# Optimization experiments

Hardware: AMD Instinct MI355X
Metric: run time of the kernel (lower is better)

## Reference

```python
import jax, jax.numpy as jnp
import numpy as np

HID, H, D = 128, 4, 32
NB, NP, NC = 60000, 2000, 4000
EM, EP, EI = 150000, 300000, 150000


def segment_softmax(logits, seg, n):
    # logits: [E, H], seg: [E] destination ids
    m = jax.ops.segment_max(logits, seg, num_segments=n)
    m = jnp.where(jnp.isfinite(m), m, 0.0)  # guard empty segments
    e = jnp.exp(logits - m[seg])
    s = jax.ops.segment_sum(e, seg, num_segments=n)
    return e / (s[seg] + 1e-16)


def layer_norm(x, g, b):
    mu = x.mean(-1, keepdims=True)
    v = ((x - mu) ** 2).mean(-1, keepdims=True)
    return (x - mu) / jnp.sqrt(v + 1e-5) * g + b


def setup_inputs():
    key = jax.random.key(0)
    ks = jax.random.split(key, 40)
    i = iter(range(40))
    nrm = lambda shape, s=1.0: jax.random.normal(ks[next(i)], shape, jnp.float32) * s
    w = lambda shape: nrm(shape, 0.05)
    inp = {
        'x_ball': nrm((NB, HID)),
        'x_player': nrm((NP, HID)),
        'x_context': nrm((NC, HID)),
        'em': jnp.stack([jax.random.randint(ks[next(i)], (EM,), 0, NP),
                         jax.random.randint(ks[next(i)], (EM,), 0, NB)]),
        'ep': jnp.stack([jax.random.randint(ks[next(i)], (EP,), 0, NB),
                         jax.random.randint(ks[next(i)], (EP,), 0, NB)]),
        'ei': jnp.stack([jax.random.randint(ks[next(i)], (EI,), 0, NB),
                         jax.random.randint(ks[next(i)], (EI,), 0, NC)]),
        'ea_p': nrm((EP, 1)),
        # GATv2Conv (player -matchup-> ball)
        'g_Wl': w((HID, HID)), 'g_Wr': w((HID, HID)), 'g_att': w((H, D)), 'g_b': jnp.zeros((HID,), jnp.float32),
        # TransformerConv (ball -recent_precedes-> ball), edge_dim=1
        't_Wq': w((HID, HID)), 't_bq': jnp.zeros((HID,), jnp.float32),
        't_Wk': w((HID, HID)), 't_bk': jnp.zeros((HID,), jnp.float32),
        't_Wv': w((HID, HID)), 't_bv': jnp.zeros((HID,), jnp.float32),
        't_We': w((1, HID)),
        't_Wskip': w((HID, HID)), 't_bskip': jnp.zeros((HID,), jnp.float32),
        # SAGEConv mean (ball -informs-> context)
        's_Wl': w((HID, HID)), 's_bl': jnp.zeros((HID,), jnp.float32), 's_Wr': w((HID, HID)),
        # per-type LayerNorms (only applied to types produced by the conv)
        'ln_ball_g': jnp.ones((HID,), jnp.float32), 'ln_ball_b': jnp.zeros((HID,), jnp.float32),
        'ln_ctx_g': jnp.ones((HID,), jnp.float32), 'ln_ctx_b': jnp.zeros((HID,), jnp.float32),
    }
    return inp


def reference(x_ball, x_player, x_context, em, ep, ei, ea_p,
              g_Wl, g_Wr, g_att, g_b,
              t_Wq, t_bq, t_Wk, t_bk, t_Wv, t_bv, t_We, t_Wskip, t_bskip,
              s_Wl, s_bl, s_Wr,
              ln_ball_g, ln_ball_b, ln_ctx_g, ln_ctx_b):
    # ---- GATv2Conv: player -> ball ----
    src, dst = em[0], em[1]
    xl = (x_player @ g_Wl).reshape(NP, H, D)   # src transform
    xr = (x_ball @ g_Wr).reshape(NB, H, D)     # dst transform
    e = xl[src] + xr[dst]                      # [EM, H, D]
    e = jnp.where(e > 0, e, 0.2 * e)           # leaky_relu(0.2)
    logit = jnp.einsum('ehd,hd->eh', e, g_att)
    alpha = segment_softmax(logit, dst, NB)
    gat = jax.ops.segment_sum(xl[src] * alpha[..., None], dst, num_segments=NB)
    gat = gat.reshape(NB, HID) + g_b

    # ---- TransformerConv: ball -> ball, edge_dim=1 ----
    src, dst = ep[0], ep[1]
    q = (x_ball @ t_Wq + t_bq).reshape(NB, H, D)
    k = (x_ball @ t_Wk + t_bk).reshape(NB, H, D)
    v = (x_ball @ t_Wv + t_bv).reshape(NB, H, D)
    ee = (ea_p @ t_We).reshape(EP, H, D)       # lin_edge (no bias)
    kj = k[src] + ee
    logit = jnp.einsum('ehd,ehd->eh', q[dst], kj) / jnp.sqrt(jnp.float32(D))
    alpha = segment_softmax(logit, dst, NB)
    tr = jax.ops.segment_sum((v[src] + ee) * alpha[..., None], dst, num_segments=NB)
    tr = tr.reshape(NB, HID) + x_ball @ t_Wskip + t_bskip  # root/skip connection

    # ---- SAGEConv mean: ball -> context ----
    src, dst = ei[0], ei[1]
    summ = jax.ops.segment_sum(x_ball[src], dst, num_segments=NC)
    cnt = jax.ops.segment_sum(jnp.ones((EI,), jnp.float32), dst, num_segments=NC)
    mean = summ / jnp.maximum(cnt, 1.0)[:, None]
    sage = mean @ s_Wl + s_bl + x_context @ s_Wr

    # ---- HeteroConv aggr='sum' + residual + per-type LayerNorm ----
    ball_out = layer_norm(gat + tr + x_ball, ln_ball_g, ln_ball_b)
    ctx_out = layer_norm(sage + x_context, ln_ctx_g, ln_ctx_b)
    # 'player' receives no messages -> passed through unchanged
    return (ball_out, ctx_out, x_player)
```

## Files before the change

### kernel.cpp

```cpp
#include <hip/hip_runtime.h>
#include <hip/hip_bf16.h>

#define NB 60000
#define NP 2000
#define NC 4000
#define EM_N 150000
#define EP_N 300000
#define EI_N 150000
#define POOL_N (EM_N + EP_N + EI_N)
#define SEG_TOT (NB + NB + NC)
#define SCAN_BLK 1024
#define NPART ((SEG_TOT + SCAN_BLK - 1) / SCAN_BLK)
#define BALL_BLKS ((NB + 127) / 128)
#define PLYR_BLKS ((NP + 127) / 128)
#define GEMM_BLKS (BALL_BLKS + PLYR_BLKS)
#define FILL_BLKS ((POOL_N + 255) / 256)
#define COPY_BLKS ((NP * 128 + 255) / 256)
#define BBALL ((NB + 3) / 4)
#define CTX_BLKS ((NC + 15) / 16)

typedef __hip_bfloat16 bf16;
typedef unsigned int u32;
typedef __attribute__((ext_vector_type(8))) short s8v;
typedef __attribute__((ext_vector_type(4))) float f4v;

__device__ __forceinline__ short f2bs(float f) {
    bf16 h = __float2bfloat16(f);
    return __builtin_bit_cast(short, h);
}
__device__ __forceinline__ float bsToF(short s) {
    return __builtin_bit_cast(float, ((unsigned)(unsigned short)s) << 16);
}
__device__ __forceinline__ float loF(u32 v) { return bsToF((short)(v & 0xffff)); }
__device__ __forceinline__ float hiF(u32 v) { return bsToF((short)(v >> 16)); }
__device__ __forceinline__ u32 packbf(float a, float b) {
    return (u32)(unsigned short)f2bs(a) | ((u32)(unsigned short)f2bs(b) << 16);
}

__global__ void hist_wt_copy_kernel(const int* __restrict__ em, const int* __restrict__ ep,
                                    const int* __restrict__ ei, int* __restrict__ counts,
                                    const float* __restrict__ W0, const float* __restrict__ W1,
                                    const float* __restrict__ W2, const float* __restrict__ W3,
                                    const float* __restrict__ W4, const float* __restrict__ W5,
                                    ushort* __restrict__ Wt,
                                    const float* __restrict__ x_player, float* __restrict__ out) {
    if (blockIdx.x >= FILL_BLKS) {
        int t = (blockIdx.x - FILL_BLKS) * 256 + threadIdx.x;
        if (t < NP * 128) out[(size_t)(NB + NC) * 128 + t] = x_player[t];
        return;
    }
    int t = blockIdx.x * 256 + threadIdx.x;
    if (t < 6 * 16384) {
        int w = t >> 14, r = t & 16383, k = r >> 7, n = r & 127;
        const float* W = (w == 0) ? W0 : (w == 1) ? W1 : (w == 2) ? W2 : (w == 3) ? W3
                       : (w == 4) ? W4 : W5;
        int sc = (n >> 5) * 32 + ((n & 1) << 4) + ((n & 31) >> 1);
        Wt[w * 16384 + sc * 128 + k] = (unsigned short)f2bs(W[k * 128 + n]);
    }
    if (t < EM_N) atomicAdd(&counts[em[EM_N + t]], 1);
    else if (t < EM_N + EP_N) atomicAdd(&counts[NB + ep[EP_N + (t - EM_N)]], 1);
    else if (t < POOL_N) atomicAdd(&counts[2 * NB + ei[EI_N + (t - EM_N - EP_N)]], 1);
}

__global__ void scan_fused_kernel(const int* __restrict__ counts, int* __restrict__ offsets,
                                  int* __restrict__ cursors, int* __restrict__ gbase) {
    __shared__ int sd[256];
    __shared__ int sbase;
    int b = blockIdx.x, tid = threadIdx.x;
    int base = b * SCAN_BLK + tid * 4;
    int v[4]; int ts = 0;
#pragma unroll
    for (int j = 0; j < 4; j++) { int idx = base + j; v[j] = (idx < SEG_TOT) ? counts[idx] : 0; ts += v[j]; }
    sd[tid] = ts;
    for (int off = 1; off < 256; off <<= 1) {
        __syncthreads(); int t = (tid >= off) ? sd[tid - off] : 0;
        __syncthreads(); sd[tid] += t;
    }
    __syncthreads();
    if (tid == 255) sbase = atomicAdd(gbase, sd[255]);
    __syncthreads();
    int run = sd[tid] - ts + sbase;
#pragma unroll
    for (int j = 0; j < 4; j++) {
        int idx = base + j;
        if (idx < SEG_TOT) { offsets[idx] = run; cursors[idx] = run; }
        run += v[j];
    }
}

__global__ __launch_bounds__(256) void gemm6_fill_kernel(
    const float* __restrict__ Aball, const float* __restrict__ Aplyr,
    const ushort* __restrict__ Wt,
    const float* __restrict__ bq, const float* __restrict__ bk,
    const float* __restrict__ bv_, const float* __restrict__ bskip,
    const float* __restrict__ g_b,
    u32* __restrict__ xrP, u32* __restrict__ qP, u32* __restrict__ kvP,
    u32* __restrict__ skipP, u32* __restrict__ xlP,
    const int* __restrict__ em, const int* __restrict__ ep, const int* __restrict__ ei,
    const float* __restrict__ ea_p, int* __restrict__ cursors, int2* __restrict__ pool) {
    if (blockIdx.x >= GEMM_BLKS) {
        int t = (blockIdx.x - GEMM_BLKS) * 256 + threadIdx.x;
        int seg, s; float ea = 0.f;
        if (t < EM_N) { s = em[t]; seg = em[EM_N + t]; }
        else if (t < EM_N + EP_N) { int e = t - EM_N; s = ep[e]; seg = NB + ep[EP_N + e]; ea = ea_p[e]; }
        else if (t < POOL_N) { int e = t - EM_N - EP_N; s = ei[e]; seg = 2 * NB + ei[EI_N + e]; }
        else return;
        int pos = atomicAdd(&cursors[seg], 1);
        pool[pos] = make_int2(s, __float_as_int(ea));
        return;
    }
    const int lane = threadIdx.x & 63;
    const int wv = threadIdx.x >> 6;
    const int quad = lane >> 4, l16 = lane & 15;
    const bool plyr = (blockIdx.x >= BALL_BLKS);
    const int M = plyr ? NP : NB;
    const float* A = plyr ? Aplyr : Aball;
    const int mbase = (plyr ? (blockIdx.x - BALL_BLKS) : blockIdx.x) * 128 + wv * 32;

    s8v a[2][4];
#pragma unroll
    for (int mt = 0; mt < 2; mt++) {
        int row = mbase + mt * 16 + l16;
        if (row >= M) row = M - 1;
        const float* ap = A + (size_t)row * 128 + quad * 8;
#pragma unroll
        for (int kt = 0; kt < 4; kt++) {
            const float4* p = (const float4*)(ap + kt * 32);
            float4 u = p[0], v = p[1];
            s8v f;
            f[0] = f2bs(u.x); f[1] = f2bs(u.y); f[2] = f2bs(u.z); f[3] = f2bs(u.w);
            f[4] = f2bs(v.x); f[5] = f2bs(v.y); f[6] = f2bs(v.z); f[7] = f2bs(v.w);
            a[mt][kt] = f;
        }
    }

    const int wbeg = plyr ? 5 : 0, wend = plyr ? 6 : 5;
    for (int w = wbeg; w < wend; w++) {
        const ushort* wt = Wt + w * 16384;
        u32* op; const float* bp; int stride, obase;
        if (w == 0)      { op = xrP;   bp = nullptr; stride = 64;  obase = 0; }
        else if (w == 1) { op = qP;    bp = bq;      stride = 64;  obase = 0; }
        else if (w == 2) { op = kvP;   bp = bk;      stride = 128; obase = 0; }
        else if (w == 3) { op = kvP;   bp = bv_;     stride = 128; obase = 1; }
        else if (w == 4) { op = skipP; bp = bskip;   stride = 64;  obase = 0; }
        else             { op = xlP;   bp = nullptr; stride = 64;  obase = 0; }
        const int kvmul = (stride == 128) ? 2 : 1;
        const bool resid = (w == 4);
#pragma unroll
        for (int t = 0; t < 4; t++) {
            s8v blo[4], bhi[4];
#pragma unroll
            for (int kt = 0; kt < 4; kt++) {
                blo[kt] = *(const s8v*)(wt + (t * 32 + l16) * 128 + kt * 32 + quad * 8);
                bhi[kt] = *(const s8v*)(wt + (t * 32 + 16 + l16) * 128 + kt * 32 + quad * 8);
            }
            float bvlo = 0.f, bvhi = 0.f;
            if (bp) { float2 b2 = ((const float2*)bp)[t * 16 + l16]; bvlo = b2.x; bvhi = b2.y; }
            if (resid) { float2 gb2 = ((const float2*)g_b)[t * 16 + l16]; bvlo += gb2.x; bvhi += gb2.y; }
#pragma unroll
            for (int mt = 0; mt < 2; mt++) {
                f4v alo = {0.f, 0.f, 0.f, 0.f}, ahi = {0.f, 0.f, 0.f, 0.f};
#pragma unroll
                for (int kt = 0; kt < 4; kt++) {
                    alo = __builtin_amdgcn_mfma_f32_16x16x32_bf16(a[mt][kt], blo[kt], alo, 0, 0, 0);
                    ahi = __builtin_amdgcn_mfma_f32_16x16x32_bf16(a[mt][kt], bhi[kt], ahi, 0, 0, 0);
                }
#pragma unroll
                for (int r = 0; r < 4; r++) {
                    int row = mbase + mt * 16 + quad * 4 + r;
                    if (row < M) {
                        float vlo = alo[r] + bvlo, vhi = ahi[r] + bvhi;
                        if (resid) {
                            float2 xr2 = ((const float2*)Aball)[(size_t)row * 64 + t * 16 + l16];
                            vlo += xr2.x; vhi += xr2.y;
                        }
                        op[(size_t)row * stride + (t * 16 + l16) * kvmul + obase] = packbf(vlo, vhi);
                    }
                }
            }
        }
    }
}

__global__ __launch_bounds__(256) void ball_sage_kernel(
    const u32* __restrict__ xlP, const u32* __restrict__ xrP, const u32* __restrict__ qP,
    const u32* __restrict__ kvP, const u32* __restrict__ skipP,
    const float* __restrict__ x_ball,
    const float* __restrict__ g_att, const float* __restrict__ We,
    const int* __restrict__ offsets, const int* __restrict__ counts,
    const int2* __restrict__ pool,
    const float* __restrict__ ln_g, const float* __restrict__ ln_b,
    float* __restrict__ summ, float* __restrict__ out) {
    __shared__ float part[4][128];
    const int wv = threadIdx.x >> 6, l = threadIdx.x & 63;

    if (blockIdx.x >= BBALL) {
        int c = blockIdx.x - BBALL;
        int beg = offsets[2 * NB + c], cnt = counts[2 * NB + c];
        float s0 = 0.f, s1 = 0.f;
        for (int j = wv; j < cnt; j += 4) {
            int s = pool[beg + j].x;
            float2 xv = ((const float2*)x_ball)[(size_t)s * 64 + l];
            s0 += xv.x; s1 += xv.y;
        }
        part[wv][l * 2] = s0; part[wv][l * 2 + 1] = s1;
        __syncthreads();
        if (wv == 0) {
            float m = fmaxf((float)cnt, 1.f);
            size_t rowC = (size_t)c * 128;
            summ[rowC + l * 2] = (part[0][l * 2] + part[1][l * 2] + part[2][l * 2] + part[3][l * 2]) / m;
            summ[rowC + l * 2 + 1] =
                (part[0][l * 2 + 1] + part[1][l * 2 + 1] + part[2][l * 2 + 1] + part[3][l * 2 + 1]) / m;
        }
        return;
    }

    const int d = blockIdx.x * 4 + wv;
    if (d >= NB) return;
    const size_t rowD = (size_t)d * 64;

    float2 att = ((const float2*)g_att)[l];
    u32 xr2 = xrP[rowD + l];
    float xr0 = loF(xr2), xr1 = hiF(xr2);
    int beg = offsets[d], cnt = counts[d];
    float n0 = 0.f, n1 = 0.f, deg = 0.f;
    int j = 0;
    for (; j + 3 < cnt; j += 4) {
        int s0 = pool[beg + j].x, s1 = pool[beg + j + 1].x;
        int s2 = pool[beg + j + 2].x, s3 = pool[beg + j + 3].x;
        u32 xv[4] = {xlP[(size_t)s0 * 64 + l], xlP[(size_t)s1 * 64 + l],
                     xlP[(size_t)s2 * 64 + l], xlP[(size_t)s3 * 64 + l]};
        float p[4], xa[4], xb[4];
#pragma unroll
        for (int i = 0; i < 4; i++) {
            xa[i] = loF(xv[i]); xb[i] = hiF(xv[i]);
            float u0 = xa[i] + xr0; u0 = u0 > 0.f ? u0 : 0.2f * u0;
            float u1 = xb[i] + xr1; u1 = u1 > 0.f ? u1 : 0.2f * u1;
            p[i] = u0 * att.x + u1 * att.y;
        }
#pragma unroll
        for (int m = 1; m <= 8; m <<= 1) {
#pragma unroll
            for (int i = 0; i < 4; i++) p[i] += __shfl_xor(p[i], m);
        }
#pragma unroll
        for (int i = 0; i < 4; i++) {
            p[i] = __expf(p[i]);
            n0 += p[i] * xa[i]; n1 += p[i] * xb[i]; deg += p[i];
        }
    }
    for (; j < cnt; j++) {
        int s = pool[beg + j].x;
        u32 xv = xlP[(size_t)s * 64 + l];
        float x0 = loF(xv), x1 = hiF(xv);
        float u0 = x0 + xr0; u0 = u0 > 0.f ? u0 : 0.2f * u0;
        float u1 = x1 + xr1; u1 = u1 > 0.f ? u1 : 0.2f * u1;
        float p = u0 * att.x + u1 * att.y;
#pragma unroll
        for (int m = 1; m <= 8; m <<= 1) p += __shfl_xor(p, m);
        p = __expf(p);
        n0 += p * x0; n1 += p * x1; deg += p;
    }
    float gat0 = n0 / (deg + 1e-16f), gat1 = n1 / (deg + 1e-16f);

    u32 q2 = qP[rowD + l];
    float q0 = loF(q2), q1 = hiF(q2);
    float2 we = ((const float2*)We)[l];
    float dw = q0 * we.x + q1 * we.y;
#pragma unroll
    for (int m = 1; m <= 8; m <<= 1) dw += __shfl_xor(dw, m);
    beg = offsets[NB + d]; cnt = counts[NB + d];
    float sv0 = 0.f, sv1 = 0.f, spe = 0.f, det = 0.f;
    const uint2* kv2p = (const uint2*)kvP;
    j = 0;
    for (; j + 3 < cnt; j += 4) {
        int2 pr[4] = {pool[beg + j], pool[beg + j + 1], pool[beg + j + 2], pool[beg + j + 3]};
        uint2 kv[4];
#pragma unroll
        for (int i = 0; i < 4; i++) kv[i] = kv2p[(size_t)pr[i].x * 64 + l];
        float p[4], ea[4];
#pragma unroll
        for (int i = 0; i < 4; i++) {
            ea[i] = __int_as_float(pr[i].y);
            p[i] = q0 * loF(kv[i].x) + q1 * hiF(kv[i].x);
        }
#pragma unroll
        for (int m = 1; m <= 8; m <<= 1) {
#pragma unroll
            for (int i = 0; i < 4; i++) p[i] += __shfl_xor(p[i], m);
        }
#pragma unroll
        for (int i = 0; i < 4; i++) {
            p[i] = __expf((p[i] + ea[i] * dw) * 0.17677669529663687f);
            sv0 += p[i] * loF(kv[i].y); sv1 += p[i] * hiF(kv[i].y);
            spe += p[i] * ea[i]; det += p[i];
        }
    }
    for (; j < cnt; j++) {
        int2 pr = pool[beg + j];
        float ea = __int_as_float(pr.y);
        uint2 kv = kv2p[(size_t)pr.x * 64 + l];
        float p = q0 * loF(kv.x) + q1 * hiF(kv.x);
#pragma unroll
        for (int m = 1; m <= 8; m <<= 1) p += __shfl_xor(p, m);
        p = __expf((p + ea * dw) * 0.17677669529663687f);
        sv0 += p * loF(kv.y); sv1 += p * hiF(kv.y);
        spe += p * ea; det += p;
    }
    float tr0 = (sv0 + spe * we.x) / (det + 1e-16f);
    float tr1 = (sv1 + spe * we.y) / (det + 1e-16f);

    u32 sk = skipP[rowD + l];
    float val0 = loF(sk) + gat0 + tr0;
    float val1 = hiF(sk) + gat1 + tr1;
    float s = val0 + val1;
#pragma unroll
    for (int m = 1; m <= 32; m <<= 1) s += __shfl_xor(s, m);
    float mu = s * (1.f / 128.f);
    float d0 = val0 - mu, d1 = val1 - mu;
    float qv = d0 * d0 + d1 * d1;
#pragma unroll
    for (int m = 1; m <= 32; m <<= 1) qv += __shfl_xor(qv, m);
    float inv = rsqrtf(qv * (1.f / 128.f) + 1e-5f);
    float2 g2 = ((const float2*)ln_g)[l];
    float2 b2 = ((const float2*)ln_b)[l];
    ((float2*)out)[rowD + l] = make_float2(d0 * inv * g2.x + b2.x, d1 * inv * g2.y + b2.y);
}

__global__ void ctx_fused_kernel(const float* __restrict__ xc, const float* __restrict__ summ,
                                 const float* __restrict__ Wr, const float* __restrict__ Wl,
                                 const float* __restrict__ bl,
                                 const float* __restrict__ g, const float* __restrict__ b,
                                 float* __restrict__ out) {
    __shared__ float A0[16 * 128];
    __shared__ float A1[16 * 128];
    __shared__ float CB[16 * 128];
    const int tid = threadIdx.x;
    const int row0 = blockIdx.x * 16;
    for (int i = tid; i < 16 * 128; i += 256) {
        int r = row0 + (i >> 7);
        A0[i] = (r < NC) ? xc[(size_t)r * 128 + (i & 127)] : 0.f;
        A1[i] = (r < NC) ? summ[(size_t)r * 128 + (i & 127)] : 0.f;
    }
    __syncthreads();
    const int col = tid & 127, rg = tid >> 7;
    float acc[8];
#pragma unroll
    for (int i = 0; i < 8; i++) acc[i] = 0.f;
    for (int k = 0; k < 128; k++) {
        float w0 = Wr[k * 128 + col], w1 = Wl[k * 128 + col];
#pragma unroll
        for (int i = 0; i < 8; i++)
            acc[i] += A0[(rg * 8 + i) * 128 + k] * w0 + A1[(rg * 8 + i) * 128 + k] * w1;
    }
    float bv = bl[col];
#pragma unroll
    for (int i = 0; i < 8; i++)
        CB[(rg * 8 + i) * 128 + col] = acc[i] + bv + A0[(rg * 8 + i) * 128 + col];
    __syncthreads();
    const int wv = tid >> 6, l = tid & 63;
    for (int r = 0; r < 4; r++) {
        int lr = wv * 4 + r, row = row0 + lr;
        if (row >= NC) break;
        float v0 = CB[lr * 128 + l], v1 = CB[lr * 128 + l + 64];
        float s = v0 + v1;
#pragma unroll
        for (int m = 1; m <= 32; m <<= 1) s += __shfl_xor(s, m);
        float mu = s * (1.f / 128.f);
        float d0 = v0 - mu, d1 = v1 - mu;
        float qv = d0 * d0 + d1 * d1;
#pragma unroll
        for (int m = 1; m <= 32; m <<= 1) qv += __shfl_xor(qv, m);
        float inv = rsqrtf(qv * (1.f / 128.f) + 1e-5f);
        out[(size_t)row * 128 + l] = d0 * inv * g[l] + b[l];
        out[(size_t)row * 128 + l + 64] = d1 * inv * g[l + 64] + b[l + 64];
    }
}

extern "C" void kernel_launch(void* const* d_in, const int* in_sizes, int n_in,
                              void* d_out, int out_size, void* d_ws, size_t ws_size,
                              hipStream_t stream) {
    const float* x_ball = (const float*)d_in[0];
    const float* x_player = (const float*)d_in[1];
    const float* x_context = (const float*)d_in[2];
    const int* em = (const int*)d_in[3];
    const int* ep = (const int*)d_in[4];
    const int* ei = (const int*)d_in[5];
    const float* ea_p = (const float*)d_in[6];
    const float* g_Wl = (const float*)d_in[7];
    const float* g_Wr = (const float*)d_in[8];
    const float* g_att = (const float*)d_in[9];
    const float* g_b = (const float*)d_in[10];
    const float* t_Wq = (const float*)d_in[11];
    const float* t_bq = (const float*)d_in[12];
    const float* t_Wk = (const float*)d_in[13];
    const float* t_bk = (const float*)d_in[14];
    const float* t_Wv = (const float*)d_in[15];
    const float* t_bv = (const float*)d_in[16];
    const float* t_We = (const float*)d_in[17];
    const float* t_Wskip = (const float*)d_in[18];
    const float* t_bskip = (const float*)d_in[19];
    const float* s_Wl = (const float*)d_in[20];
    const float* s_bl = (const float*)d_in[21];
    const float* s_Wr = (const float*)d_in[22];
    const float* ln_ball_g = (const float*)d_in[23];
    const float* ln_ball_b = (const float*)d_in[24];
    const float* ln_ctx_g = (const float*)d_in[25];
    const float* ln_ctx_b = (const float*)d_in[26];
    float* out = (float*)d_out;

    float* ws = (float*)d_ws;
    size_t o = 0;
    float* summ = ws + o;           o += (size_t)NC * 128;
    int* counts = (int*)(ws + o);   o += SEG_TOT;
    int* gbase = (int*)(ws + o);    o += 1;
    int* offsets = (int*)(ws + o);  o += SEG_TOT;
    int* cursors = (int*)(ws + o);  o += SEG_TOT;
    if (o & 1) o++;
    int2* pool = (int2*)(ws + o);   o += (size_t)POOL_N * 2;
    ushort* Wt = (ushort*)(ws + o); o += (6 * 16384) / 2;
    u32* xlP = (u32*)(ws + o);      o += (size_t)NP * 64;
    u32* xrP = (u32*)(ws + o);      o += (size_t)NB * 64;
    u32* qP = (u32*)(ws + o);       o += (size_t)NB * 64;
    u32* skipP = (u32*)(ws + o);    o += (size_t)NB * 64;
    if (o & 1) o++;
    u32* kvP = (u32*)(ws + o);      o += (size_t)NB * 128;

    dim3 blk(256);
    hipMemsetAsync(counts, 0, (SEG_TOT + 1) * sizeof(int), stream);
    hist_wt_copy_kernel<<<FILL_BLKS + COPY_BLKS, blk, 0, stream>>>(
        em, ep, ei, counts, g_Wr, t_Wq, t_Wk, t_Wv, t_Wskip, g_Wl, Wt, x_player, out);
    scan_fused_kernel<<<NPART, blk, 0, stream>>>(counts, offsets, cursors, gbase);
    gemm6_fill_kernel<<<GEMM_BLKS + FILL_BLKS, blk, 0, stream>>>(
        x_ball, x_player, Wt, t_bq, t_bk, t_bv, t_bskip, g_b,
        xrP, qP, kvP, skipP, xlP, em, ep, ei, ea_p, cursors, pool);
    ball_sage_kernel<<<BBALL + NC, blk, 0, stream>>>(
        xlP, xrP, qP, kvP, skipP, x_ball, g_att, t_We,
        offsets, counts, pool, ln_ball_g, ln_ball_b, summ, out);
    ctx_fused_kernel<<<CTX_BLKS, blk, 0, stream>>>(x_context, summ, s_Wr, s_Wl, s_bl,
                                                   ln_ctx_g, ln_ctx_b, out + (size_t)NB * 128);
}
```

Before: 334.4 us.

## Apply SAGE linear before mean aggregation and fold context GEMM into main GEMM

Since the mean is linear, this applies s_Wl to every ball row in the main MFMA GEMM, producing a bf16 xwP. It also computes x_context@s_Wr + bias + residual as a new block class in the same kernel. The SAGE gather then sums xwP rows and applies the context LayerNorm in place, which removes the separate ctx_fused kernel and its fp32 scalar GEMM. The ball gather loops are restructured into predicated groups of four with no scalar tails, and K/V are stored as a uint2 pair. The cost is one extra 60000x128 GEMM and a bf16 buffer in return for one fewer launch and half-width gathers. It also adds bf16 rounding to the SAGE path.

Measured after the change: 327.3 us. 1.02x faster.

```diff
diff --git a/kernel.cpp b/kernel.cpp
--- a/kernel.cpp
+++ b/kernel.cpp
@@ -13,11 +13,11 @@
 #define NPART ((SEG_TOT + SCAN_BLK - 1) / SCAN_BLK)
 #define BALL_BLKS ((NB + 127) / 128)
 #define PLYR_BLKS ((NP + 127) / 128)
-#define GEMM_BLKS (BALL_BLKS + PLYR_BLKS)
+#define CTXG_BLKS ((NC + 127) / 128)
+#define GEMM_BLKS (BALL_BLKS + PLYR_BLKS + CTXG_BLKS)
 #define FILL_BLKS ((POOL_N + 255) / 256)
 #define COPY_BLKS ((NP * 128 + 255) / 256)
 #define BBALL ((NB + 3) / 4)
-#define CTX_BLKS ((NC + 15) / 16)
 
 typedef __hip_bfloat16 bf16;
 typedef unsigned int u32;
@@ -42,6 +42,7 @@
                                     const float* __restrict__ W0, const float* __restrict__ W1,
                                     const float* __restrict__ W2, const float* __restrict__ W3,
                                     const float* __restrict__ W4, const float* __restrict__ W5,
+                                    const float* __restrict__ W6, const float* __restrict__ W7,
                                     ushort* __restrict__ Wt,
                                     const float* __restrict__ x_player, float* __restrict__ out) {
     if (blockIdx.x >= FILL_BLKS) {
@@ -50,10 +51,10 @@
         return;
     }
     int t = blockIdx.x * 256 + threadIdx.x;
-    if (t < 6 * 16384) {
+    if (t < 8 * 16384) {
         int w = t >> 14, r = t & 16383, k = r >> 7, n = r & 127;
         const float* W = (w == 0) ? W0 : (w == 1) ? W1 : (w == 2) ? W2 : (w == 3) ? W3
-                       : (w == 4) ? W4 : W5;
+                       : (w == 4) ? W4 : (w == 5) ? W5 : (w == 6) ? W6 : W7;
         int sc = (n >> 5) * 32 + ((n & 1) << 4) + ((n & 31) >> 1);
         Wt[w * 16384 + sc * 128 + k] = (unsigned short)f2bs(W[k * 128 + n]);
     }
@@ -88,14 +89,53 @@
     }
 }
 
+__device__ __forceinline__ void mfma_pass(const s8v a[2][4], const ushort* __restrict__ wt,
+                                          const float* __restrict__ bp, const float* __restrict__ Ares,
+                                          int mbase, int M, int l16, int quad,
+                                          u32* __restrict__ op, int stride) {
+#pragma unroll
+    for (int t = 0; t < 4; t++) {
+        s8v blo[4], bhi[4];
+#pragma unroll
+        for (int kt = 0; kt < 4; kt++) {
+            blo[kt] = *(const s8v*)(wt + (t * 32 + l16) * 128 + kt * 32 + quad * 8);
+            bhi[kt] = *(const s8v*)(wt + (t * 32 + 16 + l16) * 128 + kt * 32 + quad * 8);
+        }
+        float bvlo = 0.f, bvhi = 0.f;
+        if (bp) { float2 b2 = ((const float2*)bp)[t * 16 + l16]; bvlo = b2.x; bvhi = b2.y; }
+#pragma unroll
+        for (int mt = 0; mt < 2; mt++) {
+            f4v alo = {0.f, 0.f, 0.f, 0.f}, ahi = {0.f, 0.f, 0.f, 0.f};
+#pragma unroll
+            for (int kt = 0; kt < 4; kt++) {
+                alo = __builtin_amdgcn_mfma_f32_16x16x32_bf16(a[mt][kt], blo[kt], alo, 0, 0, 0);
+                ahi = __builtin_amdgcn_mfma_f32_16x16x32_bf16(a[mt][kt], bhi[kt], ahi, 0, 0, 0);
+            }
+#pragma unroll
+            for (int r = 0; r < 4; r++) {
+                int row = mbase + mt * 16 + quad * 4 + r;
+                if (row < M) {
+                    float vlo = alo[r] + bvlo, vhi = ahi[r] + bvhi;
+                    if (Ares) {
+                        float2 xr2 = ((const float2*)Ares)[(size_t)row * 64 + t * 16 + l16];
+                        vlo += xr2.x; vhi += xr2.y;
+                    }
+                    op[(size_t)row * stride + t * 16 + l16] = packbf(vlo, vhi);
+                }
+            }
+        }
+    }
+}
+
 __global__ __launch_bounds__(256) void gemm6_fill_kernel(
-    const float* __restrict__ Aball, const float* __restrict__ Aplyr,
+    const float* __restrict__ Aball, const float* __restrict__ Aplyr, const float* __restrict__ Actx,
     const ushort* __restrict__ Wt,
     const float* __restrict__ bq, const float* __restrict__ bk,
     const float* __restrict__ bv_, const float* __restrict__ bskip,
-    const float* __restrict__ g_b,
-    u32* __restrict__ xrP, u32* __restrict__ qP, u32* __restrict__ kvP,
-    u32* __restrict__ skipP, u32* __restrict__ xlP,
+    const float* __restrict__ g_b, const float* __restrict__ bl,
+    u32* __restrict__ xrP, u32* __restrict__ qP, uint2* __restrict__ kvP,
+    u32* __restrict__ skipP, u32* __restrict__ xlP, u32* __restrict__ xwP,
+    u32* __restrict__ ctxlinP,
     const int* __restrict__ em, const int* __restrict__ ep, const int* __restrict__ ei,
     const float* __restrict__ ea_p, int* __restrict__ cursors, int2* __restrict__ pool) {
     if (blockIdx.x >= GEMM_BLKS) {
@@ -112,10 +152,13 @@
     const int lane = threadIdx.x & 63;
     const int wv = threadIdx.x >> 6;
     const int quad = lane >> 4, l16 = lane & 15;
-    const bool plyr = (blockIdx.x >= BALL_BLKS);
-    const int M = plyr ? NP : NB;
-    const float* A = plyr ? Aplyr : Aball;
-    const int mbase = (plyr ? (blockIdx.x - BALL_BLKS) : blockIdx.x) * 128 + wv * 32;
+    int kind, bidx;
+    if (blockIdx.x < BALL_BLKS) { kind = 0; bidx = blockIdx.x; }
+    else if (blockIdx.x < BALL_BLKS + PLYR_BLKS) { kind = 1; bidx = blockIdx.x - BALL_BLKS; }
+    else { kind = 2; bidx = blockIdx.x - BALL_BLKS - PLYR_BLKS; }
+    const int M = (kind == 0) ? NB : (kind == 1) ? NP : NC;
+    const float* A = (kind == 0) ? Aball : (kind == 1) ? Aplyr : Actx;
+    const int mbase = bidx * 128 + wv * 32;
 
     s8v a[2][4];
 #pragma unroll
@@ -134,63 +177,85 @@
         }
     }
 
-    const int wbeg = plyr ? 5 : 0, wend = plyr ? 6 : 5;
-    for (int w = wbeg; w < wend; w++) {
-        const ushort* wt = Wt + w * 16384;
-        u32* op; const float* bp; int stride, obase;
-        if (w == 0)      { op = xrP;   bp = nullptr; stride = 64;  obase = 0; }
-        else if (w == 1) { op = qP;    bp = bq;      stride = 64;  obase = 0; }
-        else if (w == 2) { op = kvP;   bp = bk;      stride = 128; obase = 0; }
-        else if (w == 3) { op = kvP;   bp = bv_;     stride = 128; obase = 1; }
-        else if (w == 4) { op = skipP; bp = bskip;   stride = 64;  obase = 0; }
-        else             { op = xlP;   bp = nullptr; stride = 64;  obase = 0; }
-        const int kvmul = (stride == 128) ? 2 : 1;
-        const bool resid = (w == 4);
+    if (kind == 1) {
+        mfma_pass(a, Wt + 5 * 16384, nullptr, nullptr, mbase, M, l16, quad, xlP, 64);
+        return;
+    }
+    if (kind == 2) {
+        mfma_pass(a, Wt + 7 * 16384, bl, Actx, mbase, M, l16, quad, ctxlinP, 64);
+        return;
+    }
+    mfma_pass(a, Wt + 0 * 16384, nullptr, nullptr, mbase, M, l16, quad, xrP, 64);
+    mfma_pass(a, Wt + 1 * 16384, bq, nullptr, mbase, M, l16, quad, qP, 64);
+    {
+        const ushort* wtk = Wt + 2 * 16384;
+        const ushort* wtv = Wt + 3 * 16384;
 #pragma unroll
         for (int t = 0; t < 4; t++) {
-            s8v blo[4], bhi[4];
-#pragma unroll
-            for (int kt = 0; kt < 4; kt++) {
-                blo[kt] = *(const s8v*)(wt + (t * 32 + l16) * 128 + kt * 32 + quad * 8);
-                bhi[kt] = *(const s8v*)(wt + (t * 32 + 16 + l16) * 128 + kt * 32 + quad * 8);
+            float2 bk2 = ((const float2*)bk)[t * 16 + l16];
+            float2 bv2 = ((const float2*)bv_)[t * 16 + l16];
+            u32 kpk[2][4];
+            {
+                s8v blo[4], bhi[4];
+#pragma unroll
+                for (int kt = 0; kt < 4; kt++) {
+                    blo[kt] = *(const s8v*)(wtk + (t * 32 + l16) * 128 + kt * 32 + quad * 8);
+                    bhi[kt] = *(const s8v*)(wtk + (t * 32 + 16 + l16) * 128 + kt * 32 + quad * 8);
+                }
+#pragma unroll
+                for (int mt = 0; mt < 2; mt++) {
+                    f4v alo = {0.f, 0.f, 0.f, 0.f}, ahi = {0.f, 0.f, 0.f, 0.f};
+#pragma unroll
+                    for (int kt = 0; kt < 4; kt++) {
+                        alo = __builtin_amdgcn_mfma_f32_16x16x32_bf16(a[mt][kt], blo[kt], alo, 0, 0, 0);
+                        ahi = __builtin_amdgcn_mfma_f32_16x16x32_bf16(a[mt][kt], bhi[kt], ahi, 0, 0, 0);
+                    }
+#pragma unroll
+                    for (int r = 0; r < 4; r++)
+                        kpk[mt][r] = packbf(alo[r] + bk2.x, ahi[r] + bk2.y);
+                }
             }
-            float bvlo = 0.f, bvhi = 0.f;
-            if (bp) { float2 b2 = ((const float2*)bp)[t * 16 + l16]; bvlo = b2.x; bvhi = b2.y; }
-            if (resid) { float2 gb2 = ((const float2*)g_b)[t * 16 + l16]; bvlo += gb2.x; bvhi += gb2.y; }
-#pragma unroll
-            for (int mt = 0; mt < 2; mt++) {
-                f4v alo = {0.f, 0.f, 0.f, 0.f}, ahi = {0.f, 0.f, 0.f, 0.f};
+            {
+                s8v blo[4], bhi[4];
 #pragma unroll
                 for (int kt = 0; kt < 4; kt++) {
-                    alo = __builtin_amdgcn_mfma_f32_16x16x32_bf16(a[mt][kt], blo[kt], alo, 0, 0, 0);
-                    ahi = __builtin_amdgcn_mfma_f32_16x16x32_bf16(a[mt][kt], bhi[kt], ahi, 0, 0, 0);
+                    blo[kt] = *(const s8v*)(wtv + (t * 32 + l16) * 128 + kt * 32 + quad * 8);
+                    bhi[kt] = *(const s8v*)(wtv + (t * 32 + 16 + l16) * 128 + kt * 32 + quad * 8);
                 }
 #pragma unroll
-                for (int r = 0; r < 4; r++) {
-                    int row = mbase + mt * 16 + quad * 4 + r;
-                    if (row < M) {
-                        float vlo = alo[r] + bvlo, vhi = ahi[r] + bvhi;
-                        if (resid) {
-                            float2 xr2 = ((const float2*)Aball)[(size_t)row * 64 + t * 16 + l16];
-                            vlo += xr2.x; vhi += xr2.y;
-                        }
-                        op[(size_t)row * stride + (t * 16 + l16) * kvmul + obase] = packbf(vlo, vhi);
+                for (int mt = 0; mt < 2; mt++) {
+                    f4v alo = {0.f, 0.f, 0.f, 0.f}, ahi = {0.f, 0.f, 0.f, 0.f};
+#pragma unroll
+                    for (int kt = 0; kt < 4; kt++) {
+                        alo = __builtin_amdgcn_mfma_f32_16x16x32_bf16(a[mt][kt], blo[kt], alo, 0, 0, 0);
+                        ahi = __builtin_amdgcn_mfma_f32_16x16x32_bf16(a[mt][kt], bhi[kt], ahi, 0, 0, 0);
+                    }
+#pragma unroll
+                    for (int r = 0; r < 4; r++) {
+                        int row = mbase + mt * 16 + quad * 4 + r;
+                        if (row < NB)
+                            kvP[(size_t)row * 64 + t * 16 + l16] =
+                                make_uint2(kpk[mt][r], packbf(alo[r] + bv2.x, ahi[r] + bv2.y));
                     }
                 }
             }
         }
     }
-}
+    mfma_pass(a, Wt + 4 * 16384, bskip, Aball, mbase, M, l16, quad, skipP, 64);
+    mfma_pass(a, Wt + 6 * 16384, nullptr, nullptr, mbase, M, l16, quad, xwP, 64);
+}
+
 
 __global__ __launch_bounds__(256) void ball_sage_kernel(
     const u32* __restrict__ xlP, const u32* __restrict__ xrP, const u32* __restrict__ qP,
-    const u32* __restrict__ kvP, const u32* __restrict__ skipP,
-    const float* __restrict__ x_ball,
-    const float* __restrict__ g_att, const float* __restrict__ We,
+    const uint2* __restrict__ kvP, const u32* __restrict__ skipP, const u32* __restrict__ xwP,
+    const u32* __restrict__ ctxlinP,
+    const float* __restrict__ g_att, const float* __restrict__ g_b, const float* __restrict__ We,
     const int* __restrict__ offsets, const int* __restrict__ counts,
     const int2* __restrict__ pool,
     const float* __restrict__ ln_g, const float* __restrict__ ln_b,
-    float* __restrict__ summ, float* __restrict__ out) {
+    const float* __restrict__ cg, const float* __restrict__ cb,
+    float* __restrict__ out) {
     __shared__ float part[4][128];
     const int wv = threadIdx.x >> 6, l = threadIdx.x & 63;
 
@@ -199,24 +264,34 @@
         int beg = offsets[2 * NB + c], cnt = counts[2 * NB + c];
         float s0 = 0.f, s1 = 0.f;
         for (int j = wv; j < cnt; j += 4) {
-            int s = pool[beg + j].x;
-            float2 xv = ((const float2*)x_ball)[(size_t)s * 64 + l];
-            s0 += xv.x; s1 += xv.y;
+            u32 xv = xwP[(size_t)pool[beg + j].x * 64 + l];
+            s0 += loF(xv); s1 += hiF(xv);
         }
         part[wv][l * 2] = s0; part[wv][l * 2 + 1] = s1;
         __syncthreads();
         if (wv == 0) {
             float m = fmaxf((float)cnt, 1.f);
-            size_t rowC = (size_t)c * 128;
-            summ[rowC + l * 2] = (part[0][l * 2] + part[1][l * 2] + part[2][l * 2] + part[3][l * 2]) / m;
-            summ[rowC + l * 2 + 1] =
-                (part[0][l * 2 + 1] + part[1][l * 2 + 1] + part[2][l * 2 + 1] + part[3][l * 2 + 1]) / m;
+            u32 cl = ctxlinP[(size_t)c * 64 + l];
+            float v0 = (part[0][l * 2] + part[1][l * 2] + part[2][l * 2] + part[3][l * 2]) / m + loF(cl);
+            float v1 = (part[0][l * 2 + 1] + part[1][l * 2 + 1] + part[2][l * 2 + 1] + part[3][l * 2 + 1]) / m + hiF(cl);
+            float s = v0 + v1;
+#pragma unroll
+            for (int m2 = 1; m2 <= 32; m2 <<= 1) s += __shfl_xor(s, m2);
+            float mu = s * (1.f / 128.f);
+            float d0 = v0 - mu, d1 = v1 - mu;
+            float qv = d0 * d0 + d1 * d1;
+#pragma unroll
+            for (int m2 = 1; m2 <= 32; m2 <<= 1) qv += __shfl_xor(qv, m2);
+            float inv = rsqrtf(qv * (1.f / 128.f) + 1e-5f);
+            float2 g2 = ((const float2*)cg)[l];
+            float2 b2 = ((const float2*)cb)[l];
+            ((float2*)out)[(size_t)(NB + c) * 64 + l] =
+                make_float2(d0 * inv * g2.x + b2.x, d1 * inv * g2.y + b2.y);
         }
         return;
     }
 
     const int d = blockIdx.x * 4 + wv;
-    if (d >= NB) return;
     const size_t rowD = (size_t)d * 64;
 
     float2 att = ((const float2*)g_att)[l];
@@ -224,12 +299,16 @@
     float xr0 = loF(xr2), xr1 = hiF(xr2);
     int beg = offsets[d], cnt = counts[d];
     float n0 = 0.f, n1 = 0.f, deg = 0.f;
-    int j = 0;
-    for (; j + 3 < cnt; j += 4) {
-        int s0 = pool[beg + j].x, s1 = pool[beg + j + 1].x;
-        int s2 = pool[beg + j + 2].x, s3 = pool[beg + j + 3].x;
-        u32 xv[4] = {xlP[(size_t)s0 * 64 + l], xlP[(size_t)s1 * 64 + l],
-                     xlP[(size_t)s2 * 64 + l], xlP[(size_t)s3 * 64 + l]};
+    for (int j = 0; j < cnt; j += 4) {
+        int sI[4]; bool ok[4];
+#pragma unroll
+        for (int i = 0; i < 4; i++) {
+            ok[i] = (j + i < cnt);
+            sI[i] = ok[i] ? pool[beg + j + i].x : 0;
+        }
+        u32 xv[4];
+#pragma unroll
+        for (int i = 0; i < 4; i++) xv[i] = xlP[(size_t)sI[i] * 64 + l];
         float p[4], xa[4], xb[4];
 #pragma unroll
         for (int i = 0; i < 4; i++) {
@@ -245,21 +324,9 @@
         }
 #pragma unroll
         for (int i = 0; i < 4; i++) {
-            p[i] = __expf(p[i]);
+            p[i] = ok[i] ? __expf(p[i]) : 0.f;
             n0 += p[i] * xa[i]; n1 += p[i] * xb[i]; deg += p[i];
         }
-    }
-    for (; j < cnt; j++) {
-        int s = pool[beg + j].x;
-        u32 xv = xlP[(size_t)s * 64 + l];
-        float x0 = loF(xv), x1 = hiF(xv);
-        float u0 = x0 + xr0; u0 = u0 > 0.f ? u0 : 0.2f * u0;
-        float u1 = x1 + xr1; u1 = u1 > 0.f ? u1 : 0.2f * u1;
-        float p = u0 * att.x + u1 * att.y;
-#pragma unroll
-        for (int m = 1; m <= 8; m <<= 1) p += __shfl_xor(p, m);
-        p = __expf(p);
-        n0 += p * x0; n1 += p * x1; deg += p;
     }
     float gat0 = n0 / (deg + 1e-16f), gat1 = n1 / (deg + 1e-16f);
 
@@ -271,13 +338,16 @@
     for (int m = 1; m <= 8; m <<= 1) dw += __shfl_xor(dw, m);
     beg = offsets[NB + d]; cnt = counts[NB + d];
     float sv0 = 0.f, sv1 = 0.f, spe = 0.f, det = 0.f;
-    const uint2* kv2p = (const uint2*)kvP;
-    j = 0;
-    for (; j + 3 < cnt; j += 4) {
-        int2 pr[4] = {pool[beg + j], pool[beg + j + 1], pool[beg + j + 2], pool[beg + j + 3]};
+    for (int j = 0; j < cnt; j += 4) {
+        int2 pr[4]; bool ok[4];
+#pragma unroll
+        for (int i = 0; i < 4; i++) {
+            ok[i] = (j + i < cnt);
+            pr[i] = ok[i] ? pool[beg + j + i] : make_int2(0, 0);
+        }
         uint2 kv[4];
 #pragma unroll
-        for (int i = 0; i < 4; i++) kv[i] = kv2p[(size_t)pr[i].x * 64 + l];
+        for (int i = 0; i < 4; i++) kv[i] = kvP[(size_t)pr[i].x * 64 + l];
         float p[4], ea[4];
 #pragma unroll
         for (int i = 0; i < 4; i++) {
@@ -291,28 +361,18 @@
         }
 #pragma unroll
         for (int i = 0; i < 4; i++) {
-            p[i] = __expf((p[i] + ea[i] * dw) * 0.17677669529663687f);
+            p[i] = ok[i] ? __expf((p[i] + ea[i] * dw) * 0.17677669529663687f) : 0.f;
             sv0 += p[i] * loF(kv[i].y); sv1 += p[i] * hiF(kv[i].y);
             spe += p[i] * ea[i]; det += p[i];
         }
     }
-    for (; j < cnt; j++) {
-        int2 pr = pool[beg + j];
-        float ea = __int_as_float(pr.y);
-        uint2 kv = kv2p[(size_t)pr.x * 64 + l];
-        float p = q0 * loF(kv.x) + q1 * hiF(kv.x);
-#pragma unroll
-        for (int m = 1; m <= 8; m <<= 1) p += __shfl_xor(p, m);
-        p = __expf((p + ea * dw) * 0.17677669529663687f);
-        sv0 += p * loF(kv.y); sv1 += p * hiF(kv.y);
-        spe += p * ea; det += p;
-    }
     float tr0 = (sv0 + spe * we.x) / (det + 1e-16f);
     float tr1 = (sv1 + spe * we.y) / (det + 1e-16f);
 
     u32 sk = skipP[rowD + l];
-    float val0 = loF(sk) + gat0 + tr0;
-    float val1 = hiF(sk) + gat1 + tr1;
+    float2 gb2 = ((const float2*)g_b)[l];
+    float val0 = loF(sk) + gb2.x + gat0 + tr0;
+    float val1 = hiF(sk) + gb2.y + gat1 + tr1;
     float s = val0 + val1;
 #pragma unroll
     for (int m = 1; m <= 32; m <<= 1) s += __shfl_xor(s, m);
@@ -325,56 +385,6 @@
     float2 g2 = ((const float2*)ln_g)[l];
     float2 b2 = ((const float2*)ln_b)[l];
     ((float2*)out)[rowD + l] = make_float2(d0 * inv * g2.x + b2.x, d1 * inv * g2.y + b2.y);
-}
-
-__global__ void ctx_fused_kernel(const float* __restrict__ xc, const float* __restrict__ summ,
-                                 const float* __restrict__ Wr, const float* __restrict__ Wl,
-                                 const float* __restrict__ bl,
-                                 const float* __restrict__ g, const float* __restrict__ b,
-                                 float* __restrict__ out) {
-    __shared__ float A0[16 * 128];
-    __shared__ float A1[16 * 128];
-    __shared__ float CB[16 * 128];
-    const int tid = threadIdx.x;
-    const int row0 = blockIdx.x * 16;
-    for (int i = tid; i < 16 * 128; i += 256) {
-        int r = row0 + (i >> 7);
-        A0[i] = (r < NC) ? xc[(size_t)r * 128 + (i & 127)] : 0.f;
-        A1[i] = (r < NC) ? summ[(size_t)r * 128 + (i & 127)] : 0.f;
-    }
-    __syncthreads();
-    const int col = tid & 127, rg = tid >> 7;
-    float acc[8];
-#pragma unroll
-    for (int i = 0; i < 8; i++) acc[i] = 0.f;
-    for (int k = 0; k < 128; k++) {
-        float w0 = Wr[k * 128 + col], w1 = Wl[k * 128 + col];
-#pragma unroll
-        for (int i = 0; i < 8; i++)
-            acc[i] += A0[(rg * 8 + i) * 128 + k] * w0 + A1[(rg * 8 + i) * 128 + k] * w1;
-    }
-    float bv = bl[col];
-#pragma unroll
-    for (int i = 0; i < 8; i++)
-        CB[(rg * 8 + i) * 128 + col] = acc[i] + bv + A0[(rg * 8 + i) * 128 + col];
-    __syncthreads();
-    const int wv = tid >> 6, l = tid & 63;
-    for (int r = 0; r < 4; r++) {
-        int lr = wv * 4 + r, row = row0 + lr;
-        if (row >= NC) break;
-        float v0 = CB[lr * 128 + l], v1 = CB[lr * 128 + l + 64];
-        float s = v0 + v1;
-#pragma unroll
-        for (int m = 1; m <= 32; m <<= 1) s += __shfl_xor(s, m);
-        float mu = s * (1.f / 128.f);
-        float d0 = v0 - mu, d1 = v1 - mu;
-        float qv = d0 * d0 + d1 * d1;
-#pragma unroll
-        for (int m = 1; m <= 32; m <<= 1) qv += __shfl_xor(qv, m);
-        float inv = rsqrtf(qv * (1.f / 128.f) + 1e-5f);
-        out[(size_t)row * 128 + l] = d0 * inv * g[l] + b[l];
-        out[(size_t)row * 128 + l + 64] = d1 * inv * g[l + 64] + b[l + 64];
-    }
 }
 
 extern "C" void kernel_launch(void* const* d_in, const int* in_sizes, int n_in,
@@ -411,32 +421,31 @@
 
     float* ws = (float*)d_ws;
     size_t o = 0;
-    float* summ = ws + o;           o += (size_t)NC * 128;
     int* counts = (int*)(ws + o);   o += SEG_TOT;
     int* gbase = (int*)(ws + o);    o += 1;
     int* offsets = (int*)(ws + o);  o += SEG_TOT;
     int* cursors = (int*)(ws + o);  o += SEG_TOT;
     if (o & 1) o++;
     int2* pool = (int2*)(ws + o);   o += (size_t)POOL_N * 2;
-    ushort* Wt = (ushort*)(ws + o); o += (6 * 16384) / 2;
+    ushort* Wt = (ushort*)(ws + o); o += (8 * 16384) / 2;
     u32* xlP = (u32*)(ws + o);      o += (size_t)NP * 64;
     u32* xrP = (u32*)(ws + o);      o += (size_t)NB * 64;
     u32* qP = (u32*)(ws + o);       o += (size_t)NB * 64;
     u32* skipP = (u32*)(ws + o);    o += (size_t)NB * 64;
+    u32* xwP = (u32*)(ws + o);      o += (size_t)NB * 64;
+    u32* ctxlinP = (u32*)(ws + o);  o += (size_t)NC * 64;
     if (o & 1) o++;
-    u32* kvP = (u32*)(ws + o);      o += (size_t)NB * 128;
+    uint2* kvP = (uint2*)(ws + o);  o += (size_t)NB * 128;
 
     dim3 blk(256);
     hipMemsetAsync(counts, 0, (SEG_TOT + 1) * sizeof(int), stream);
     hist_wt_copy_kernel<<<FILL_BLKS + COPY_BLKS, blk, 0, stream>>>(
-        em, ep, ei, counts, g_Wr, t_Wq, t_Wk, t_Wv, t_Wskip, g_Wl, Wt, x_player, out);
+        em, ep, ei, counts, g_Wr, t_Wq, t_Wk, t_Wv, t_Wskip, g_Wl, s_Wl, s_Wr, Wt, x_player, out);
     scan_fused_kernel<<<NPART, blk, 0, stream>>>(counts, offsets, cursors, gbase);
     gemm6_fill_kernel<<<GEMM_BLKS + FILL_BLKS, blk, 0, stream>>>(
-        x_ball, x_player, Wt, t_bq, t_bk, t_bv, t_bskip, g_b,
-        xrP, qP, kvP, skipP, xlP, em, ep, ei, ea_p, cursors, pool);
+        x_ball, x_player, x_context, Wt, t_bq, t_bk, t_bv, t_bskip, g_b, s_bl,
+        xrP, qP, kvP, skipP, xlP, xwP, ctxlinP, em, ep, ei, ea_p, cursors, pool);
     ball_sage_kernel<<<BBALL + NC, blk, 0, stream>>>(
-        xlP, xrP, qP, kvP, skipP, x_ball, g_att, t_We,
-        offsets, counts, pool, ln_ball_g, ln_ball_b, summ, out);
-    ctx_fused_kernel<<<CTX_BLKS, blk, 0, stream>>>(x_context, summ, s_Wr, s_Wl, s_bl,
-                                                   ln_ctx_g, ln_ctx_b, out + (size_t)NB * 128);
-}
+        xlP, xrP, qP, kvP, skipP, xwP, ctxlinP, g_att, g_b, t_We,
+        offsets, counts, pool, ln_ball_g, ln_ball_b, ln_ctx_g, ln_ctx_b, out);
+}
```
